# Performance work log

Measured on AMD Instinct MI355X. Metric: run time of the kernel, lower is better.

Reference implementation:

```python
import jax, jax.numpy as jnp
import numpy as np

B, IN_DIM, LATENT = 1024, 256, 256


def _linear_params(key, fan_in, fan_out):
    # torch nn.Linear default init: U(-1/sqrt(fan_in), 1/sqrt(fan_in))
    k1, k2 = jax.random.split(key)
    lim = 1.0 / np.sqrt(fan_in)
    W = jax.random.uniform(k1, (fan_out, fan_in), minval=-lim, maxval=lim, dtype=jnp.float32)
    b = jax.random.uniform(k2, (fan_out,), minval=-lim, maxval=lim, dtype=jnp.float32)
    return W, b


def setup_inputs() -> dict:
    key = jax.random.key(0)
    ks = jax.random.split(key, 8)
    Wd1, bd1 = _linear_params(ks[0], IN_DIM, LATENT)
    Wd2, bd2 = _linear_params(ks[1], LATENT, LATENT)
    Wu1, bu1 = _linear_params(ks[2], IN_DIM, LATENT)
    Wu2, bu2 = _linear_params(ks[3], LATENT, LATENT)
    Wm1, bm1 = _linear_params(ks[4], IN_DIM, LATENT)
    Wm2, bm2 = _linear_params(ks[5], LATENT, LATENT)
    x = jax.random.normal(ks[6], (B, IN_DIM), dtype=jnp.float32)
    v = jax.random.normal(ks[7], (B, LATENT), dtype=jnp.float32)  # noise from calculate_z
    return {
        "x": x,
        "Wd1": Wd1, "bd1": bd1, "Wd2": Wd2, "bd2": bd2,
        "Wu1": Wu1, "bu1": bu1, "Wu2": Wu2, "bu2": bu2,
        "Wm1": Wm1, "bm1": bm1, "Wm2": Wm2, "bm2": bm2,
        "v": v,
    }


def reference(x, Wd1, bd1, Wd2, bd2, Wu1, bu1, Wu2, bu2, Wm1, bm1, Wm2, bm2, v):
    sig = jax.nn.sigmoid
    # three small 2-layer MLPs
    d = sig(sig(x @ Wd1.T + bd1) @ Wd2.T + bd2)          # [B, n]
    u = sig(sig(x @ Wu1.T + bu1) @ Wu2.T + bu2)          # [B, n]
    mean = jnp.tanh(jnp.tanh(x @ Wm1.T + bm1) @ Wm2.T + bm2)  # [B, n]

    # calculate_r: inverse of diag_embed(d) is diag(1/d); +epsilon is added to ALL
    # entries (as in the original torch code), making D_inv a full matrix.
    EPS = 1e-6
    n = d.shape[-1]
    eye = jnp.eye(n, dtype=d.dtype)
    D_inv = (1.0 / d)[..., None] * eye + EPS               # [B, n, n]
    D_in_sqr = jnp.sqrt(D_inv)                             # elementwise sqrt
    U = u[:, :, None] * u[:, None, :]                      # rank-1 [B, n, n]
    ut_d_inv_u = jnp.einsum('bi,bij,bj->b', u, D_inv, u)[:, None, None]  # [B,1,1]
    eta = 1.0 / (1.0 + ut_d_inv_u)
    right = (1.0 - jnp.sqrt(eta)) / ut_d_inv_u
    R = D_in_sqr - right * jnp.matmul(D_inv, jnp.matmul(U, D_in_sqr))  # [B, n, n]

    # calculate_z
    z = jnp.einsum('bij,bj->bi', R, v) + mean              # [B, n]
    return (mean, R, z)
```

## Files before the change

### kernel.cpp

```cpp
#include <hip/hip_runtime.h>
#include <hip/hip_bf16.h>
#include <math.h>

#define NB 1024
#define N 256
#define EPS 1e-6f
#define SQRT_EPS 1e-3f

typedef short bf16x8 __attribute__((ext_vector_type(8)));
typedef float f32x4  __attribute__((ext_vector_type(4)));

__device__ __forceinline__ float fast_rcp(float x) {
    return __builtin_amdgcn_rcpf(x);
}
__device__ __forceinline__ float sigmoidf(float x) {
    return fast_rcp(1.0f + __expf(-x));
}
__device__ __forceinline__ float fast_tanh(float x) {
    float ax = fabsf(x);
    float e  = __expf(2.0f * ax);
    float t  = 1.0f - 2.0f * fast_rcp(e + 1.0f);
    return copysignf(t, x);
}
__device__ __forceinline__ unsigned short to_bf16(float f) {
    __hip_bfloat16 h = __float2bfloat16(f);
    return *(unsigned short*)&h;
}

__global__ __launch_bounds__(256) void prep_kernel(
    const float* __restrict__ Wd1, const float* __restrict__ Wu1,
    const float* __restrict__ Wm1, const float* __restrict__ Wd2,
    const float* __restrict__ Wu2, const float* __restrict__ Wm2,
    unsigned short* __restrict__ out)
{
    const int fi = blockIdx.x * 256 + threadIdx.x;
    const int r  = fi >> 14;
    const int off = (fi & 16383) * 4;
    const float* src = (r == 0) ? Wd1 : (r == 1) ? Wu1 : (r == 2) ? Wm1
                     : (r == 3) ? Wd2 : (r == 4) ? Wu2 : Wm2;
    float4 f = *(const float4*)(src + off);
    ushort4 o;
    o.x = to_bf16(f.x); o.y = to_bf16(f.y); o.z = to_bf16(f.z); o.w = to_bf16(f.w);
    *(ushort4*)(out + r * 65536 + off) = o;
}

__global__ __launch_bounds__(256) void l1_kernel(
    const float* __restrict__ x, const unsigned short* __restrict__ Wb,
    const float* __restrict__ bd1, const float* __restrict__ bu1,
    const float* __restrict__ bm1, unsigned short* __restrict__ h1g)
{
    const int tid = threadIdx.x;
    const int w   = tid >> 6;
    const int l   = tid & 63;
    const int ml  = l & 15;
    const int kg  = l >> 4;
    const int b0  = (blockIdx.x >> 2) * 16;
    const int n0  = (blockIdx.x & 3) * 64 + w * 16;

    bf16x8 af[8];
    {
        const float* xrow = x + (size_t)(b0 + ml) * N;
        #pragma unroll
        for (int kq = 0; kq < 8; ++kq) {
            float4 f0 = *(const float4*)(xrow + kq * 32 + kg * 8);
            float4 f1 = *(const float4*)(xrow + kq * 32 + kg * 8 + 4);
            bf16x8 a;
            a[0] = (short)to_bf16(f0.x); a[1] = (short)to_bf16(f0.y);
            a[2] = (short)to_bf16(f0.z); a[3] = (short)to_bf16(f0.w);
            a[4] = (short)to_bf16(f1.x); a[5] = (short)to_bf16(f1.y);
            a[6] = (short)to_bf16(f1.z); a[7] = (short)to_bf16(f1.w);
            af[kq] = a;
        }
    }
    #pragma unroll
    for (int mlp = 0; mlp < 3; ++mlp) {
        const unsigned short* Wl = Wb + (size_t)mlp * 65536;
        f32x4 acc = {0.f, 0.f, 0.f, 0.f};
        #pragma unroll
        for (int kq = 0; kq < 8; ++kq) {
            bf16x8 bf = *(const bf16x8*)(Wl + (size_t)(n0 + ml) * N + kq * 32 + kg * 8);
            acc = __builtin_amdgcn_mfma_f32_16x16x32_bf16(af[kq], bf, acc, 0, 0, 0);
        }
        const float* bias = (mlp == 0) ? bd1 : (mlp == 1) ? bu1 : bm1;
        const int n = n0 + ml;
        const float bb = bias[n];
        #pragma unroll
        for (int reg = 0; reg < 4; ++reg) {
            const int row = b0 + kg * 4 + reg;
            float val = acc[reg] + bb;
            float act = (mlp < 2) ? sigmoidf(val) : fast_tanh(val);
            h1g[(size_t)mlp * (NB * N) + (size_t)row * N + n] = to_bf16(act);
        }
    }
}

__global__ __launch_bounds__(256) void l2_kernel(
    const unsigned short* __restrict__ h1g, const unsigned short* __restrict__ Wb,
    const float* __restrict__ bd2, const float* __restrict__ bu2,
    const float* __restrict__ bm2, float* __restrict__ h2g)
{
    const int tid = threadIdx.x;
    const int w   = tid >> 6;
    const int l   = tid & 63;
    const int ml  = l & 15;
    const int kg  = l >> 6 == 0 ? (l >> 4) : (l >> 4);
    const int b0  = (blockIdx.x >> 2) * 16;
    const int n0  = (blockIdx.x & 3) * 64 + w * 16;

    #pragma unroll
    for (int mlp = 0; mlp < 3; ++mlp) {
        const unsigned short* arow = h1g + (size_t)mlp * (NB * N) + (size_t)(b0 + ml) * N;
        bf16x8 af[8];
        #pragma unroll
        for (int kq = 0; kq < 8; ++kq)
            af[kq] = *(const bf16x8*)(arow + kq * 32 + (l >> 4) * 8);
        const unsigned short* Wl = Wb + (size_t)(3 + mlp) * 65536;
        f32x4 acc = {0.f, 0.f, 0.f, 0.f};
        #pragma unroll
        for (int kq = 0; kq < 8; ++kq) {
            bf16x8 bf = *(const bf16x8*)(Wl + (size_t)(n0 + ml) * N + kq * 32 + (l >> 4) * 8);
            acc = __builtin_amdgcn_mfma_f32_16x16x32_bf16(af[kq], bf, acc, 0, 0, 0);
        }
        const float* bias = (mlp == 0) ? bd2 : (mlp == 1) ? bu2 : bm2;
        const int n = n0 + ml;
        const float bb = bias[n];
        #pragma unroll
        for (int reg = 0; reg < 4; ++reg) {
            const int row = b0 + (l >> 4) * 4 + reg;
            float val = acc[reg] + bb;
            float act = (mlp < 2) ? sigmoidf(val) : fast_tanh(val);
            h2g[(size_t)mlp * (NB * N) + (size_t)row * N + n] = act;
        }
    }
}

__global__ __launch_bounds__(256) void epi_kernel(
    const float* __restrict__ h2g, const float* __restrict__ v,
    float* __restrict__ out_mean, float* __restrict__ out_z,
    float* __restrict__ ws_a, float* __restrict__ ws_tp, float* __restrict__ ws_s)
{
    const int tid = threadIdx.x;
    const int w   = tid >> 6;
    const int l   = tid & 63;
    const int row = blockIdx.x * 4 + w;

    float dd[4], uu[4], vv[4];
    float Su = 0.f, qs = 0.f, Sv = 0.f;
    #pragma unroll
    for (int c = 0; c < 4; ++c) {
        const int n = l + 64 * c;
        dd[c] = h2g[(size_t)0 * (NB * N) + (size_t)row * N + n];
        uu[c] = h2g[(size_t)1 * (NB * N) + (size_t)row * N + n];
        vv[c] = v[(size_t)row * N + n];
        Su += uu[c];
        qs += uu[c] * uu[c] * fast_rcp(dd[c]);
        Sv += vv[c];
    }
    #pragma unroll
    for (int off = 1; off < 64; off <<= 1) {
        Su += __shfl_xor(Su, off, 64);
        qs += __shfl_xor(qs, off, 64);
        Sv += __shfl_xor(Sv, off, 64);
    }
    const float utDu  = qs + EPS * Su * Su;
    const float sqeta = rsqrtf(1.0f + utDu);
    const float right = (1.0f - sqeta) / utDu;

    float aC[4], tpC[4], sC[4];
    float sv = 0.f;
    #pragma unroll
    for (int c = 0; c < 4; ++c) {
        const float inv_d = fast_rcp(dd[c]);
        aC[c]  = sqrtf(inv_d + EPS);
        sC[c]  = uu[c] * aC[c] + SQRT_EPS * (Su - uu[c]);
        tpC[c] = right * (uu[c] * inv_d + EPS * Su);
        sv += sC[c] * vv[c];
    }
    #pragma unroll
    for (int off = 1; off < 64; off <<= 1)
        sv += __shfl_xor(sv, off, 64);

    #pragma unroll
    for (int c = 0; c < 4; ++c) {
        const int n = l + 64 * c;
        const size_t idx = (size_t)row * N + n;
        const float m_ = h2g[(size_t)2 * (NB * N) + idx];
        out_mean[idx] = m_;
        out_z[idx]    = SQRT_EPS * Sv + (aC[c] - SQRT_EPS) * vv[c] - tpC[c] * sv + m_;
        ws_a[idx]     = aC[c];
        ws_tp[idx]    = tpC[c];
        ws_s[idx]     = sC[c];
    }
}

__global__ __launch_bounds__(256) void r_kernel(
    const float* __restrict__ ws_a, const float* __restrict__ ws_tp,
    const float* __restrict__ ws_s, float* __restrict__ R)
{
    __shared__ float s_lds[N];
    __shared__ float a_lds[64];
    __shared__ float tp_lds[64];

    const int tid   = threadIdx.x;
    const int b     = blockIdx.x >> 2;
    const int chunk = blockIdx.x & 3;
    const int ibase = chunk * 64;

    s_lds[tid] = ws_s[(size_t)b * N + tid];
    if (tid < 64) {
        a_lds[tid]  = ws_a[(size_t)b * N + ibase + tid];
        tp_lds[tid] = ws_tp[(size_t)b * N + ibase + tid];
    }
    __syncthreads();

    const int j4 = tid & 63;
    const int il = tid >> 6;
    const float4 sv = ((const float4*)s_lds)[j4];
    float4* Rb = (float4*)(R + (size_t)b * N * N);
    const int jb = j4 * 4;

    #pragma unroll
    for (int it = 0; it < 16; ++it) {
        const int i_loc = it * 4 + il;
        const int i     = ibase + i_loc;
        const float a   = a_lds[i_loc];
        const float tp  = tp_lds[i_loc];
        float4 o;
        o.x = SQRT_EPS - tp * sv.x;
        o.y = SQRT_EPS - tp * sv.y;
        o.z = SQRT_EPS - tp * sv.z;
        o.w = SQRT_EPS - tp * sv.w;
        if (i >= jb && i < jb + 4) {
            const float add = a - SQRT_EPS;
            if      (i == jb)     o.x += add;
            else if (i == jb + 1) o.y += add;
            else if (i == jb + 2) o.z += add;
            else                  o.w += add;
        }
        Rb[(size_t)i * 64 + j4] = o;
    }
}

extern "C" void kernel_launch(void* const* d_in, const int* in_sizes, int n_in,
                              void* d_out, int out_size, void* d_ws, size_t ws_size,
                              hipStream_t stream) {
    const float* x   = (const float*)d_in[0];
    const float* Wd1 = (const float*)d_in[1];
    const float* bd1 = (const float*)d_in[2];
    const float* Wd2 = (const float*)d_in[3];
    const float* bd2 = (const float*)d_in[4];
    const float* Wu1 = (const float*)d_in[5];
    const float* bu1 = (const float*)d_in[6];
    const float* Wu2 = (const float*)d_in[7];
    const float* bu2 = (const float*)d_in[8];
    const float* Wm1 = (const float*)d_in[9];
    const float* bm1 = (const float*)d_in[10];
    const float* Wm2 = (const float*)d_in[11];
    const float* bm2 = (const float*)d_in[12];
    const float* v   = (const float*)d_in[13];

    float* out      = (float*)d_out;
    float* out_mean = out;
    float* R        = out + (size_t)NB * N;
    float* out_z    = R + (size_t)NB * N * N;

    float* wsf   = (float*)d_ws;
    float* ws_a  = wsf;
    float* ws_tp = wsf + (size_t)NB * N;
    float* ws_s  = wsf + (size_t)2 * NB * N;
    unsigned short* Wb  = (unsigned short*)(wsf + (size_t)3 * NB * N);
    unsigned short* h1g = Wb + 6 * 65536;
    float* h2g = (float*)(h1g + 3 * NB * N);

    prep_kernel<<<384, 256, 0, stream>>>(Wd1, Wu1, Wm1, Wd2, Wu2, Wm2, Wb);

    l1_kernel<<<256, 256, 0, stream>>>(x, Wb, bd1, bu1, bm1, h1g);
    l2_kernel<<<256, 256, 0, stream>>>(h1g, Wb, bd2, bu2, bm2, h2g);
    epi_kernel<<<256, 256, 0, stream>>>(h2g, v, out_mean, out_z, ws_a, ws_tp, ws_s);

    r_kernel<<<NB * 4, 256, 0, stream>>>(ws_a, ws_tp, ws_s, R);
}
```

Before: 70.40 us.

## Fuse both MLP layers and epilogue into one LDS-staged kernel

Merges the layer-1, layer-2 and epilogue kernels into a single 1024-thread block per 16 batch rows. Hidden activations are kept in shared memory instead of being written to and read back from global buffers. This removes two kernel launches and the intermediate global traffic. In exchange the grid shrinks to 64 blocks, which may underuse the GPU's compute units, and the kernel needs a large LDS footprint.

```diff
diff --git a/kernel.cpp b/kernel.cpp
--- a/kernel.cpp
+++ b/kernel.cpp
@@ -44,18 +44,26 @@
     *(ushort4*)(out + r * 65536 + off) = o;
 }
 
-__global__ __launch_bounds__(256) void l1_kernel(
+#define H1S 264
+__global__ __launch_bounds__(1024) void mlp_fused_kernel(
     const float* __restrict__ x, const unsigned short* __restrict__ Wb,
     const float* __restrict__ bd1, const float* __restrict__ bu1,
-    const float* __restrict__ bm1, unsigned short* __restrict__ h1g)
+    const float* __restrict__ bm1, const float* __restrict__ bd2,
+    const float* __restrict__ bu2, const float* __restrict__ bm2,
+    const float* __restrict__ v,
+    float* __restrict__ out_mean, float* __restrict__ out_z,
+    float* __restrict__ ws_a, float* __restrict__ ws_tp, float* __restrict__ ws_s)
 {
+    __shared__ unsigned short h1s[3][16][H1S];
+    __shared__ float h2f[3][16][H1S];
+
     const int tid = threadIdx.x;
     const int w   = tid >> 6;
     const int l   = tid & 63;
     const int ml  = l & 15;
     const int kg  = l >> 4;
-    const int b0  = (blockIdx.x >> 2) * 16;
-    const int n0  = (blockIdx.x & 3) * 64 + w * 16;
+    const int b0  = blockIdx.x * 16;
+    const int n0  = w * 16;
 
     bf16x8 af[8];
     {
@@ -86,110 +94,89 @@
         const float bb = bias[n];
         #pragma unroll
         for (int reg = 0; reg < 4; ++reg) {
-            const int row = b0 + kg * 4 + reg;
+            const int row = kg * 4 + reg;
             float val = acc[reg] + bb;
             float act = (mlp < 2) ? sigmoidf(val) : fast_tanh(val);
-            h1g[(size_t)mlp * (NB * N) + (size_t)row * N + n] = to_bf16(act);
-        }
-    }
-}
-
-__global__ __launch_bounds__(256) void l2_kernel(
-    const unsigned short* __restrict__ h1g, const unsigned short* __restrict__ Wb,
-    const float* __restrict__ bd2, const float* __restrict__ bu2,
-    const float* __restrict__ bm2, float* __restrict__ h2g)
-{
-    const int tid = threadIdx.x;
-    const int w   = tid >> 6;
-    const int l   = tid & 63;
-    const int ml  = l & 15;
-    const int kg  = l >> 6 == 0 ? (l >> 4) : (l >> 4);
-    const int b0  = (blockIdx.x >> 2) * 16;
-    const int n0  = (blockIdx.x & 3) * 64 + w * 16;
+            h1s[mlp][row][n] = to_bf16(act);
+        }
+    }
+    __syncthreads();
 
     #pragma unroll
     for (int mlp = 0; mlp < 3; ++mlp) {
-        const unsigned short* arow = h1g + (size_t)mlp * (NB * N) + (size_t)(b0 + ml) * N;
-        bf16x8 af[8];
+        bf16x8 af2[8];
         #pragma unroll
         for (int kq = 0; kq < 8; ++kq)
-            af[kq] = *(const bf16x8*)(arow + kq * 32 + (l >> 4) * 8);
+            af2[kq] = *(const bf16x8*)&h1s[mlp][ml][kq * 32 + kg * 8];
         const unsigned short* Wl = Wb + (size_t)(3 + mlp) * 65536;
         f32x4 acc = {0.f, 0.f, 0.f, 0.f};
         #pragma unroll
         for (int kq = 0; kq < 8; ++kq) {
-            bf16x8 bf = *(const bf16x8*)(Wl + (size_t)(n0 + ml) * N + kq * 32 + (l >> 4) * 8);
-            acc = __builtin_amdgcn_mfma_f32_16x16x32_bf16(af[kq], bf, acc, 0, 0, 0);
+            bf16x8 bf = *(const bf16x8*)(Wl + (size_t)(n0 + ml) * N + kq * 32 + kg * 8);
+            acc = __builtin_amdgcn_mfma_f32_16x16x32_bf16(af2[kq], bf, acc, 0, 0, 0);
         }
         const float* bias = (mlp == 0) ? bd2 : (mlp == 1) ? bu2 : bm2;
         const int n = n0 + ml;
         const float bb = bias[n];
         #pragma unroll
         for (int reg = 0; reg < 4; ++reg) {
-            const int row = b0 + (l >> 4) * 4 + reg;
+            const int row = kg * 4 + reg;
             float val = acc[reg] + bb;
             float act = (mlp < 2) ? sigmoidf(val) : fast_tanh(val);
-            h2g[(size_t)mlp * (NB * N) + (size_t)row * N + n] = act;
-        }
-    }
-}
-
-__global__ __launch_bounds__(256) void epi_kernel(
-    const float* __restrict__ h2g, const float* __restrict__ v,
-    float* __restrict__ out_mean, float* __restrict__ out_z,
-    float* __restrict__ ws_a, float* __restrict__ ws_tp, float* __restrict__ ws_s)
-{
-    const int tid = threadIdx.x;
-    const int w   = tid >> 6;
-    const int l   = tid & 63;
-    const int row = blockIdx.x * 4 + w;
-
-    float dd[4], uu[4], vv[4];
-    float Su = 0.f, qs = 0.f, Sv = 0.f;
-    #pragma unroll
-    for (int c = 0; c < 4; ++c) {
-        const int n = l + 64 * c;
-        dd[c] = h2g[(size_t)0 * (NB * N) + (size_t)row * N + n];
-        uu[c] = h2g[(size_t)1 * (NB * N) + (size_t)row * N + n];
-        vv[c] = v[(size_t)row * N + n];
-        Su += uu[c];
-        qs += uu[c] * uu[c] * fast_rcp(dd[c]);
-        Sv += vv[c];
-    }
-    #pragma unroll
-    for (int off = 1; off < 64; off <<= 1) {
-        Su += __shfl_xor(Su, off, 64);
-        qs += __shfl_xor(qs, off, 64);
-        Sv += __shfl_xor(Sv, off, 64);
-    }
-    const float utDu  = qs + EPS * Su * Su;
-    const float sqeta = rsqrtf(1.0f + utDu);
-    const float right = (1.0f - sqeta) / utDu;
-
-    float aC[4], tpC[4], sC[4];
-    float sv = 0.f;
-    #pragma unroll
-    for (int c = 0; c < 4; ++c) {
-        const float inv_d = fast_rcp(dd[c]);
-        aC[c]  = sqrtf(inv_d + EPS);
-        sC[c]  = uu[c] * aC[c] + SQRT_EPS * (Su - uu[c]);
-        tpC[c] = right * (uu[c] * inv_d + EPS * Su);
-        sv += sC[c] * vv[c];
-    }
-    #pragma unroll
-    for (int off = 1; off < 64; off <<= 1)
-        sv += __shfl_xor(sv, off, 64);
-
-    #pragma unroll
-    for (int c = 0; c < 4; ++c) {
-        const int n = l + 64 * c;
-        const size_t idx = (size_t)row * N + n;
-        const float m_ = h2g[(size_t)2 * (NB * N) + idx];
-        out_mean[idx] = m_;
-        out_z[idx]    = SQRT_EPS * Sv + (aC[c] - SQRT_EPS) * vv[c] - tpC[c] * sv + m_;
-        ws_a[idx]     = aC[c];
-        ws_tp[idx]    = tpC[c];
-        ws_s[idx]     = sC[c];
+            h2f[mlp][row][n] = act;
+        }
+    }
+    __syncthreads();
+
+    {
+        const int r = w;
+        float dd[4], uu[4], vv[4];
+        float Su = 0.f, qs = 0.f, Sv = 0.f;
+        #pragma unroll
+        for (int c = 0; c < 4; ++c) {
+            const int n = l + 64 * c;
+            dd[c] = h2f[0][r][n];
+            uu[c] = h2f[1][r][n];
+            vv[c] = v[(size_t)(b0 + r) * N + n];
+            Su += uu[c];
+            qs += uu[c] * uu[c] * fast_rcp(dd[c]);
+            Sv += vv[c];
+        }
+        #pragma unroll
+        for (int off = 1; off < 64; off <<= 1) {
+            Su += __shfl_xor(Su, off, 64);
+            qs += __shfl_xor(qs, off, 64);
+            Sv += __shfl_xor(Sv, off, 64);
+        }
+        const float utDu  = qs + EPS * Su * Su;
+        const float sqeta = rsqrtf(1.0f + utDu);
+        const float right = (1.0f - sqeta) / utDu;
+
+        float aC[4], tpC[4], sC[4];
+        float sv = 0.f;
+        #pragma unroll
+        for (int c = 0; c < 4; ++c) {
+            const float inv_d = fast_rcp(dd[c]);
+            aC[c]  = sqrtf(inv_d + EPS);
+            sC[c]  = uu[c] * aC[c] + SQRT_EPS * (Su - uu[c]);
+            tpC[c] = right * (uu[c] * inv_d + EPS * Su);
+            sv += sC[c] * vv[c];
+        }
+        #pragma unroll
+        for (int off = 1; off < 64; off <<= 1)
+            sv += __shfl_xor(sv, off, 64);
+
+        #pragma unroll
+        for (int c = 0; c < 4; ++c) {
+            const int n = l + 64 * c;
+            const size_t idx = (size_t)(b0 + r) * N + n;
+            const float m_ = h2f[2][r][n];
+            out_mean[idx] = m_;
+            out_z[idx]    = SQRT_EPS * Sv + (aC[c] - SQRT_EPS) * vv[c] - tpC[c] * sv + m_;
+            ws_a[idx]     = aC[c];
+            ws_tp[idx]    = tpC[c];
+            ws_s[idx]     = sC[c];
+        }
     }
 }
 
@@ -268,15 +255,13 @@
     float* ws_a  = wsf;
     float* ws_tp = wsf + (size_t)NB * N;
     float* ws_s  = wsf + (size_t)2 * NB * N;
-    unsigned short* Wb  = (unsigned short*)(wsf + (size_t)3 * NB * N);
-    unsigned short* h1g = Wb + 6 * 65536;
-    float* h2g = (float*)(h1g + 3 * NB * N);
+    unsigned short* Wb = (unsigned short*)(wsf + (size_t)3 * NB * N);
 
     prep_kernel<<<384, 256, 0, stream>>>(Wd1, Wu1, Wm1, Wd2, Wu2, Wm2, Wb);
 
-    l1_kernel<<<256, 256, 0, stream>>>(x, Wb, bd1, bu1, bm1, h1g);
-    l2_kernel<<<256, 256, 0, stream>>>(h1g, Wb, bd2, bu2, bm2, h2g);
-    epi_kernel<<<256, 256, 0, stream>>>(h2g, v, out_mean, out_z, ws_a, ws_tp, ws_s);
+    mlp_fused_kernel<<<NB / 16, 1024, 0, stream>>>(
+        x, Wb, bd1, bu1, bm1, bd2, bu2, bm2, v,
+        out_mean, out_z, ws_a, ws_tp, ws_s);
 
     r_kernel<<<NB * 4, 256, 0, stream>>>(ws_a, ws_tp, ws_s, R);
 }
```

Result: slower. 84.64 us (+20.2%).

## Fuse weight conversion into GEMMs, split MLPs across waves, merge epilogue into R kernel

Applied to the files above, without the earlier changes.

Removes the separate weight-to-bf16 prep kernel; the layer kernels now read fp32 weights and convert them in-register. Each layer kernel runs 768 threads, with one group of four waves per MLP, so the three MLPs run in parallel instead of in a serial loop. The epilogue is merged into the R-writing kernel, which recomputes the per-row reductions in every one of the four chunk blocks. This cuts two launches and the workspace round trip for a, tp and s, at the cost of redundant reductions and more fp32 weight traffic.

```diff
diff --git a/kernel.cpp b/kernel.cpp
--- a/kernel.cpp
+++ b/kernel.cpp
@@ -4,6 +4,7 @@
 
 #define NB 1024
 #define N 256
+#define NBN (NB * N)
 #define EPS 1e-6f
 #define SQRT_EPS 1e-3f
 
@@ -26,36 +27,32 @@
     __hip_bfloat16 h = __float2bfloat16(f);
     return *(unsigned short*)&h;
 }
-
-__global__ __launch_bounds__(256) void prep_kernel(
+__device__ __forceinline__ bf16x8 cvt8(float4 f0, float4 f1) {
+    bf16x8 a;
+    a[0] = (short)to_bf16(f0.x); a[1] = (short)to_bf16(f0.y);
+    a[2] = (short)to_bf16(f0.z); a[3] = (short)to_bf16(f0.w);
+    a[4] = (short)to_bf16(f1.x); a[5] = (short)to_bf16(f1.y);
+    a[6] = (short)to_bf16(f1.z); a[7] = (short)to_bf16(f1.w);
+    return a;
+}
+
+__global__ __launch_bounds__(768) void l1_kernel(
+    const float* __restrict__ x,
     const float* __restrict__ Wd1, const float* __restrict__ Wu1,
-    const float* __restrict__ Wm1, const float* __restrict__ Wd2,
-    const float* __restrict__ Wu2, const float* __restrict__ Wm2,
-    unsigned short* __restrict__ out)
-{
-    const int fi = blockIdx.x * 256 + threadIdx.x;
-    const int r  = fi >> 14;
-    const int off = (fi & 16383) * 4;
-    const float* src = (r == 0) ? Wd1 : (r == 1) ? Wu1 : (r == 2) ? Wm1
-                     : (r == 3) ? Wd2 : (r == 4) ? Wu2 : Wm2;
-    float4 f = *(const float4*)(src + off);
-    ushort4 o;
-    o.x = to_bf16(f.x); o.y = to_bf16(f.y); o.z = to_bf16(f.z); o.w = to_bf16(f.w);
-    *(ushort4*)(out + r * 65536 + off) = o;
-}
-
-__global__ __launch_bounds__(256) void l1_kernel(
-    const float* __restrict__ x, const unsigned short* __restrict__ Wb,
+    const float* __restrict__ Wm1,
     const float* __restrict__ bd1, const float* __restrict__ bu1,
     const float* __restrict__ bm1, unsigned short* __restrict__ h1g)
 {
     const int tid = threadIdx.x;
     const int w   = tid >> 6;
+    const int mlp = w >> 2;
+    const int sub = w & 3;
     const int l   = tid & 63;
     const int ml  = l & 15;
     const int kg  = l >> 4;
     const int b0  = (blockIdx.x >> 2) * 16;
-    const int n0  = (blockIdx.x & 3) * 64 + w * 16;
+    const int n0  = (blockIdx.x & 3) * 64 + sub * 16;
+    const int n   = n0 + ml;
 
     bf16x8 af[8];
     {
@@ -64,158 +61,142 @@
         for (int kq = 0; kq < 8; ++kq) {
             float4 f0 = *(const float4*)(xrow + kq * 32 + kg * 8);
             float4 f1 = *(const float4*)(xrow + kq * 32 + kg * 8 + 4);
-            bf16x8 a;
-            a[0] = (short)to_bf16(f0.x); a[1] = (short)to_bf16(f0.y);
-            a[2] = (short)to_bf16(f0.z); a[3] = (short)to_bf16(f0.w);
-            a[4] = (short)to_bf16(f1.x); a[5] = (short)to_bf16(f1.y);
-            a[6] = (short)to_bf16(f1.z); a[7] = (short)to_bf16(f1.w);
-            af[kq] = a;
+            af[kq] = cvt8(f0, f1);
         }
     }
-    #pragma unroll
-    for (int mlp = 0; mlp < 3; ++mlp) {
-        const unsigned short* Wl = Wb + (size_t)mlp * 65536;
-        f32x4 acc = {0.f, 0.f, 0.f, 0.f};
-        #pragma unroll
-        for (int kq = 0; kq < 8; ++kq) {
-            bf16x8 bf = *(const bf16x8*)(Wl + (size_t)(n0 + ml) * N + kq * 32 + kg * 8);
-            acc = __builtin_amdgcn_mfma_f32_16x16x32_bf16(af[kq], bf, acc, 0, 0, 0);
-        }
-        const float* bias = (mlp == 0) ? bd1 : (mlp == 1) ? bu1 : bm1;
-        const int n = n0 + ml;
-        const float bb = bias[n];
-        #pragma unroll
-        for (int reg = 0; reg < 4; ++reg) {
-            const int row = b0 + kg * 4 + reg;
-            float val = acc[reg] + bb;
-            float act = (mlp < 2) ? sigmoidf(val) : fast_tanh(val);
-            h1g[(size_t)mlp * (NB * N) + (size_t)row * N + n] = to_bf16(act);
-        }
-    }
-}
-
-__global__ __launch_bounds__(256) void l2_kernel(
-    const unsigned short* __restrict__ h1g, const unsigned short* __restrict__ Wb,
+    const float* Wl = (mlp == 0) ? Wd1 : (mlp == 1) ? Wu1 : Wm1;
+    const float* wrow = Wl + (size_t)n * N;
+    f32x4 acc = {0.f, 0.f, 0.f, 0.f};
+    #pragma unroll
+    for (int kq = 0; kq < 8; ++kq) {
+        float4 f0 = *(const float4*)(wrow + kq * 32 + kg * 8);
+        float4 f1 = *(const float4*)(wrow + kq * 32 + kg * 8 + 4);
+        bf16x8 bf = cvt8(f0, f1);
+        acc = __builtin_amdgcn_mfma_f32_16x16x32_bf16(af[kq], bf, acc, 0, 0, 0);
+    }
+    const float* bias = (mlp == 0) ? bd1 : (mlp == 1) ? bu1 : bm1;
+    const float bb = bias[n];
+    #pragma unroll
+    for (int reg = 0; reg < 4; ++reg) {
+        const int row = b0 + kg * 4 + reg;
+        float val = acc[reg] + bb;
+        float act = (mlp < 2) ? sigmoidf(val) : fast_tanh(val);
+        h1g[(size_t)mlp * NBN + (size_t)row * N + n] = to_bf16(act);
+    }
+}
+
+__global__ __launch_bounds__(768) void l2_kernel(
+    const unsigned short* __restrict__ h1g,
+    const float* __restrict__ Wd2, const float* __restrict__ Wu2,
+    const float* __restrict__ Wm2,
     const float* __restrict__ bd2, const float* __restrict__ bu2,
     const float* __restrict__ bm2, float* __restrict__ h2g)
 {
     const int tid = threadIdx.x;
     const int w   = tid >> 6;
+    const int mlp = w >> 2;
+    const int sub = w & 3;
     const int l   = tid & 63;
     const int ml  = l & 15;
-    const int kg  = l >> 6 == 0 ? (l >> 4) : (l >> 4);
+    const int kg  = l >> 4;
     const int b0  = (blockIdx.x >> 2) * 16;
-    const int n0  = (blockIdx.x & 3) * 64 + w * 16;
-
-    #pragma unroll
-    for (int mlp = 0; mlp < 3; ++mlp) {
-        const unsigned short* arow = h1g + (size_t)mlp * (NB * N) + (size_t)(b0 + ml) * N;
-        bf16x8 af[8];
+    const int n0  = (blockIdx.x & 3) * 64 + sub * 16;
+    const int n   = n0 + ml;
+
+    bf16x8 af[8];
+    {
+        const unsigned short* arow = h1g + (size_t)mlp * NBN + (size_t)(b0 + ml) * N;
         #pragma unroll
         for (int kq = 0; kq < 8; ++kq)
-            af[kq] = *(const bf16x8*)(arow + kq * 32 + (l >> 4) * 8);
-        const unsigned short* Wl = Wb + (size_t)(3 + mlp) * 65536;
-        f32x4 acc = {0.f, 0.f, 0.f, 0.f};
-        #pragma unroll
-        for (int kq = 0; kq < 8; ++kq) {
-            bf16x8 bf = *(const bf16x8*)(Wl + (size_t)(n0 + ml) * N + kq * 32 + (l >> 4) * 8);
-            acc = __builtin_amdgcn_mfma_f32_16x16x32_bf16(af[kq], bf, acc, 0, 0, 0);
-        }
-        const float* bias = (mlp == 0) ? bd2 : (mlp == 1) ? bu2 : bm2;
-        const int n = n0 + ml;
-        const float bb = bias[n];
-        #pragma unroll
-        for (int reg = 0; reg < 4; ++reg) {
-            const int row = b0 + (l >> 4) * 4 + reg;
-            float val = acc[reg] + bb;
-            float act = (mlp < 2) ? sigmoidf(val) : fast_tanh(val);
-            h2g[(size_t)mlp * (NB * N) + (size_t)row * N + n] = act;
-        }
-    }
-}
-
-__global__ __launch_bounds__(256) void epi_kernel(
+            af[kq] = *(const bf16x8*)(arow + kq * 32 + kg * 8);
+    }
+    const float* Wl = (mlp == 0) ? Wd2 : (mlp == 1) ? Wu2 : Wm2;
+    const float* wrow = Wl + (size_t)n * N;
+    f32x4 acc = {0.f, 0.f, 0.f, 0.f};
+    #pragma unroll
+    for (int kq = 0; kq < 8; ++kq) {
+        float4 f0 = *(const float4*)(wrow + kq * 32 + kg * 8);
+        float4 f1 = *(const float4*)(wrow + kq * 32 + kg * 8 + 4);
+        bf16x8 bf = cvt8(f0, f1);
+        acc = __builtin_amdgcn_mfma_f32_16x16x32_bf16(af[kq], bf, acc, 0, 0, 0);
+    }
+    const float* bias = (mlp == 0) ? bd2 : (mlp == 1) ? bu2 : bm2;
+    const float bb = bias[n];
+    #pragma unroll
+    for (int reg = 0; reg < 4; ++reg) {
+        const int row = b0 + kg * 4 + reg;
+        float val = acc[reg] + bb;
+        float act = (mlp < 2) ? sigmoidf(val) : fast_tanh(val);
+        h2g[(size_t)mlp * NBN + (size_t)row * N + n] = act;
+    }
+}
+
+__global__ __launch_bounds__(256) void r_epi_kernel(
     const float* __restrict__ h2g, const float* __restrict__ v,
     float* __restrict__ out_mean, float* __restrict__ out_z,
-    float* __restrict__ ws_a, float* __restrict__ ws_tp, float* __restrict__ ws_s)
-{
-    const int tid = threadIdx.x;
-    const int w   = tid >> 6;
-    const int l   = tid & 63;
-    const int row = blockIdx.x * 4 + w;
-
-    float dd[4], uu[4], vv[4];
-    float Su = 0.f, qs = 0.f, Sv = 0.f;
-    #pragma unroll
-    for (int c = 0; c < 4; ++c) {
-        const int n = l + 64 * c;
-        dd[c] = h2g[(size_t)0 * (NB * N) + (size_t)row * N + n];
-        uu[c] = h2g[(size_t)1 * (NB * N) + (size_t)row * N + n];
-        vv[c] = v[(size_t)row * N + n];
-        Su += uu[c];
-        qs += uu[c] * uu[c] * fast_rcp(dd[c]);
-        Sv += vv[c];
-    }
-    #pragma unroll
-    for (int off = 1; off < 64; off <<= 1) {
-        Su += __shfl_xor(Su, off, 64);
-        qs += __shfl_xor(qs, off, 64);
-        Sv += __shfl_xor(Sv, off, 64);
-    }
-    const float utDu  = qs + EPS * Su * Su;
-    const float sqeta = rsqrtf(1.0f + utDu);
-    const float right = (1.0f - sqeta) / utDu;
-
-    float aC[4], tpC[4], sC[4];
-    float sv = 0.f;
-    #pragma unroll
-    for (int c = 0; c < 4; ++c) {
-        const float inv_d = fast_rcp(dd[c]);
-        aC[c]  = sqrtf(inv_d + EPS);
-        sC[c]  = uu[c] * aC[c] + SQRT_EPS * (Su - uu[c]);
-        tpC[c] = right * (uu[c] * inv_d + EPS * Su);
-        sv += sC[c] * vv[c];
-    }
-    #pragma unroll
-    for (int off = 1; off < 64; off <<= 1)
-        sv += __shfl_xor(sv, off, 64);
-
-    #pragma unroll
-    for (int c = 0; c < 4; ++c) {
-        const int n = l + 64 * c;
-        const size_t idx = (size_t)row * N + n;
-        const float m_ = h2g[(size_t)2 * (NB * N) + idx];
-        out_mean[idx] = m_;
-        out_z[idx]    = SQRT_EPS * Sv + (aC[c] - SQRT_EPS) * vv[c] - tpC[c] * sv + m_;
-        ws_a[idx]     = aC[c];
-        ws_tp[idx]    = tpC[c];
-        ws_s[idx]     = sC[c];
-    }
-}
-
-__global__ __launch_bounds__(256) void r_kernel(
-    const float* __restrict__ ws_a, const float* __restrict__ ws_tp,
-    const float* __restrict__ ws_s, float* __restrict__ R)
+    float* __restrict__ R)
 {
     __shared__ float s_lds[N];
     __shared__ float a_lds[64];
     __shared__ float tp_lds[64];
+    __shared__ float red1[4][3];
+    __shared__ float red2[4];
 
     const int tid   = threadIdx.x;
     const int b     = blockIdx.x >> 2;
     const int chunk = blockIdx.x & 3;
     const int ibase = chunk * 64;
-
-    s_lds[tid] = ws_s[(size_t)b * N + tid];
-    if (tid < 64) {
-        a_lds[tid]  = ws_a[(size_t)b * N + ibase + tid];
-        tp_lds[tid] = ws_tp[(size_t)b * N + ibase + tid];
-    }
+    const int lane  = tid & 63;
+    const int wv    = tid >> 6;
+
+    const float d_ = h2g[(size_t)0 * NBN + (size_t)b * N + tid];
+    const float u_ = h2g[(size_t)1 * NBN + (size_t)b * N + tid];
+    const float m_ = h2g[(size_t)2 * NBN + (size_t)b * N + tid];
+    const float vv = v[(size_t)b * N + tid];
+    const float inv_d = fast_rcp(d_);
+
+    float s0 = u_, s1 = u_ * u_ * inv_d, s2 = vv;
+    #pragma unroll
+    for (int off = 32; off > 0; off >>= 1) {
+        s0 += __shfl_down(s0, off, 64);
+        s1 += __shfl_down(s1, off, 64);
+        s2 += __shfl_down(s2, off, 64);
+    }
+    if (lane == 0) { red1[wv][0] = s0; red1[wv][1] = s1; red1[wv][2] = s2; }
     __syncthreads();
+    const float Su = red1[0][0] + red1[1][0] + red1[2][0] + red1[3][0];
+    const float qs = red1[0][1] + red1[1][1] + red1[2][1] + red1[3][1];
+    const float Sv = red1[0][2] + red1[1][2] + red1[2][2] + red1[3][2];
+    const float utDu  = qs + EPS * Su * Su;
+    const float sqeta = rsqrtf(1.0f + utDu);
+    const float right = (1.0f - sqeta) / utDu;
+    const float a  = sqrtf(inv_d + EPS);
+    const float s  = u_ * a + SQRT_EPS * (Su - u_);
+    const float tp = right * (u_ * inv_d + EPS * Su);
+
+    float sv = s * vv;
+    #pragma unroll
+    for (int off = 32; off > 0; off >>= 1)
+        sv += __shfl_down(sv, off, 64);
+    if (lane == 0) red2[wv] = sv;
+
+    s_lds[tid] = s;
+    if (tid >= ibase && tid < ibase + 64) {
+        a_lds[tid - ibase]  = a;
+        tp_lds[tid - ibase] = tp;
+    }
+    __syncthreads();
+    sv = red2[0] + red2[1] + red2[2] + red2[3];
+
+    if (chunk == 0) {
+        const size_t idx = (size_t)b * N + tid;
+        out_mean[idx] = m_;
+        out_z[idx]    = SQRT_EPS * Sv + (a - SQRT_EPS) * vv - tp * sv + m_;
+    }
 
     const int j4 = tid & 63;
     const int il = tid >> 6;
-    const float4 sv = ((const float4*)s_lds)[j4];
+    const float4 svec = ((const float4*)s_lds)[j4];
     float4* Rb = (float4*)(R + (size_t)b * N * N);
     const int jb = j4 * 4;
 
@@ -223,15 +204,15 @@
     for (int it = 0; it < 16; ++it) {
         const int i_loc = it * 4 + il;
         const int i     = ibase + i_loc;
-        const float a   = a_lds[i_loc];
-        const float tp  = tp_lds[i_loc];
+        const float ai  = a_lds[i_loc];
+        const float ti  = tp_lds[i_loc];
         float4 o;
-        o.x = SQRT_EPS - tp * sv.x;
-        o.y = SQRT_EPS - tp * sv.y;
-        o.z = SQRT_EPS - tp * sv.z;
-        o.w = SQRT_EPS - tp * sv.w;
+        o.x = SQRT_EPS - ti * svec.x;
+        o.y = SQRT_EPS - ti * svec.y;
+        o.z = SQRT_EPS - ti * svec.z;
+        o.w = SQRT_EPS - ti * svec.w;
         if (i >= jb && i < jb + 4) {
-            const float add = a - SQRT_EPS;
+            const float add = ai - SQRT_EPS;
             if      (i == jb)     o.x += add;
             else if (i == jb + 1) o.y += add;
             else if (i == jb + 2) o.z += add;
@@ -264,19 +245,10 @@
     float* R        = out + (size_t)NB * N;
     float* out_z    = R + (size_t)NB * N * N;
 
-    float* wsf   = (float*)d_ws;
-    float* ws_a  = wsf;
-    float* ws_tp = wsf + (size_t)NB * N;
-    float* ws_s  = wsf + (size_t)2 * NB * N;
-    unsigned short* Wb  = (unsigned short*)(wsf + (size_t)3 * NB * N);
-    unsigned short* h1g = Wb + 6 * 65536;
-    float* h2g = (float*)(h1g + 3 * NB * N);
-
-    prep_kernel<<<384, 256, 0, stream>>>(Wd1, Wu1, Wm1, Wd2, Wu2, Wm2, Wb);
-
-    l1_kernel<<<256, 256, 0, stream>>>(x, Wb, bd1, bu1, bm1, h1g);
-    l2_kernel<<<256, 256, 0, stream>>>(h1g, Wb, bd2, bu2, bm2, h2g);
-    epi_kernel<<<256, 256, 0, stream>>>(h2g, v, out_mean, out_z, ws_a, ws_tp, ws_s);
-
-    r_kernel<<<NB * 4, 256, 0, stream>>>(ws_a, ws_tp, ws_s, R);
-}
+    unsigned short* h1g = (unsigned short*)d_ws;
+    float* h2g = (float*)(h1g + (size_t)3 * NBN);
+
+    l1_kernel<<<256, 768, 0, stream>>>(x, Wd1, Wu1, Wm1, bd1, bu1, bm1, h1g);
+    l2_kernel<<<256, 768, 0, stream>>>(h1g, Wd2, Wu2, Wm2, bd2, bu2, bm2, h2g);
+    r_epi_kernel<<<NB * 4, 256, 0, stream>>>(h2g, v, out_mean, out_z, R);
+}
```

New measurement: 72.16 us. 1.02x slower.
